# Kernel tuning notes

Hardware: AMD Instinct MI355X
Metric: run time of the kernel (lower is better)

The kernel has to match this reference:

```python
import jax, jax.numpy as jnp
import numpy as np
from jax.scipy.special import logsumexp


def setup_inputs() -> dict:
    key = jax.random.key(0)
    B, C, H, W = 2, 32, 128, 128
    sizes = [(H, W)] + [(H // 2, W // 2)] * 4
    ks = iter(jax.random.split(key, 32))
    inp = {}
    for t, (hh, ww) in enumerate(sizes):
        inp[f"unary_h{t}"] = jax.random.normal(next(ks), (B, C, hh, ww), jnp.float32)
        inp[f"unary_v{t}"] = jax.random.normal(next(ks), (B, C, hh, ww), jnp.float32)
        inp[f"pairwise_h{t}"] = 0.1 * jax.random.normal(next(ks), (B, C, C, hh, ww - 1), jnp.float32)
        inp[f"pairwise_v{t}"] = 0.1 * jax.random.normal(next(ks), (B, C, C, hh - 1, ww), jnp.float32)
    inp["gamma"] = jnp.ones((1,), jnp.float32)
    return inp


def _chain_marginals(unary, pairwise, gamma):
    """Entropy-smoothed max-product marginals along the LAST axis.
    unary: [B,C,L,T], pairwise: [B,C,C,L,T-1] (pairwise[b,i,j,l,t] couples state i at t with j at t+1).
    Returns soft marginals [B,C,L,T] (softmax over C per position)."""
    u = jnp.transpose(unary, (3, 0, 2, 1))        # [T,B,L,C]
    pw = jnp.transpose(pairwise, (4, 0, 3, 1, 2))  # [T-1,B,L,C,C]
    inv_g = 1.0 / gamma

    def fwd_step(f, xs):
        u_t, pw_t = xs
        f_new = u_t + gamma * logsumexp(f[..., :, None] * inv_g + pw_t * inv_g, axis=-2)
        return f_new, f_new

    _, f_rest = jax.lax.scan(fwd_step, u[0], (u[1:], pw))
    f = jnp.concatenate([u[:1], f_rest], axis=0)

    def bwd_step(bb, xs):
        u_t, pw_t = xs
        b_new = u_t + gamma * logsumexp(bb[..., None, :] * inv_g + pw_t * inv_g, axis=-1)
        return b_new, b_new

    _, b_rest = jax.lax.scan(bwd_step, u[-1], (u[:-1][::-1], pw[::-1]))
    b = jnp.concatenate([u[-1:], b_rest], axis=0)[::-1]

    marg = jax.nn.softmax((f + b - u) * inv_g, axis=-1)  # [T,B,L,C]
    return jnp.transpose(marg, (1, 3, 2, 0))             # [B,C,L,T]


def _dp_pair(uh, uv, ph, pv, g):
    # horizontal chains (along W) with unary_h, vertical chains (along H) with unary_v
    mh = _chain_marginals(uh, ph, g)
    mv = _chain_marginals(uv.swapaxes(2, 3), pv.swapaxes(3, 4), g).swapaxes(2, 3)
    return mh, mv


def _scatter_up(m, stride, i, j, H, W):
    # max_unpool2d with the structured indices: m[y,x] -> (i + y*stride, j + x*stride), then crop/pad to (H,W)
    b, c, h_, w_ = m.shape
    up = jnp.zeros((b, c, h_ * stride, w_ * stride), m.dtype).at[:, :, i::stride, j::stride].set(m)
    up = up[:, :, :H, :W]
    ph, pw = H - up.shape[2], W - up.shape[3]
    if ph > 0 or pw > 0:
        up = jnp.pad(up, ((0, 0), (0, 0), (0, max(ph, 0)), (0, max(pw, 0))))
    return up


def reference(unary_h0, unary_h1, unary_h2, unary_h3, unary_h4,
              unary_v0, unary_v1, unary_v2, unary_v3, unary_v4,
              pairwise_h0, pairwise_h1, pairwise_h2, pairwise_h3, pairwise_h4,
              pairwise_v0, pairwise_v1, pairwise_v2, pairwise_v3, pairwise_v4,
              gamma):
    uh = [unary_h0, unary_h1, unary_h2, unary_h3, unary_h4]
    uv = [unary_v0, unary_v1, unary_v2, unary_v3, unary_v4]
    ph = [pairwise_h0, pairwise_h1, pairwise_h2, pairwise_h3, pairwise_h4]
    pv = [pairwise_v0, pairwise_v1, pairwise_v2, pairwise_v3, pairwise_v4]
    g = jnp.clip(gamma.reshape(()), 0.01)  # learned gamma, clamped min 0.01

    H, W = uh[0].shape[2], uh[0].shape[3]
    alpha = 1.0 / W if W > H else 1.0 / H

    mh0, mv0 = _dp_pair(uh[0], uv[0], ph[0], pv[0], g)
    marg_hs, marg_vs = [mh0], [mv0]
    mh_acc, mv_acc = mh0, mv0

    stride, cnt = 2, 1  # step_size = 1 default -> one extra scale with a 2x2 shifted grid
    for i in range(stride):
        for j in range(stride):
            m_h, m_v = _dp_pair(uh[cnt], uv[cnt], ph[cnt], pv[cnt], g)
            marg_hs.append(m_h)
            marg_vs.append(m_v)
            mh_acc = mh_acc + _scatter_up(m_h, stride, i, j, H, W)
            mv_acc = mv_acc + _scatter_up(m_v, stride, i, j, H, W)
            cnt += 1

    num_pairwise_terms = 2
    avg = (mh_acc + mv_acc) / (num_pairwise_terms * 2)

    new_uh0 = uh[0] - alpha * (marg_hs[0] - avg)
    new_uv0 = uv[0] - alpha * (marg_vs[0] - avg)
    # fine-scale unary updates (computed for faithfulness; gradients flow through avg)
    cnt = 1
    new_uh_fine, new_uv_fine = [], []
    for i in range(stride):
        for j in range(stride):
            new_uh_fine.append(uh[cnt] - alpha * (marg_hs[cnt] - avg[:, :, i::stride, j::stride]))
            new_uv_fine.append(uv[cnt] - alpha * (marg_vs[cnt] - avg[:, :, i::stride, j::stride]))
            cnt += 1

    main = jnp.stack([new_uh0, new_uv0, mh_acc, mv_acc], axis=0)  # [4,B,C,H,W]
    return main
```

## Files before the change

### kernel.cpp

```cpp
#include <hip/hip_runtime.h>
#include <stdint.h>

#define TC 4
#define CHUNK_BYTES 8192
#define CHUNK_F4 512

static __device__ __forceinline__ float lse16x2(const float* v, float igl2, float gln2, float uval)
{
  float a0=fmaxf(v[0],v[8]), a1=fmaxf(v[1],v[9]), a2=fmaxf(v[2],v[10]), a3=fmaxf(v[3],v[11]);
  float a4=fmaxf(v[4],v[12]),a5=fmaxf(v[5],v[13]),a6=fmaxf(v[6],v[14]),a7=fmaxf(v[7],v[15]);
  float b0=fmaxf(a0,a4), b1=fmaxf(a1,a5), b2=fmaxf(a2,a6), b3=fmaxf(a3,a7);
  float m = fmaxf(fmaxf(b0,b1), fmaxf(b2,b3));
  float e0 = exp2f((v[0]-m)*igl2) + exp2f((v[1]-m)*igl2);
  float e1 = exp2f((v[2]-m)*igl2) + exp2f((v[3]-m)*igl2);
  float e2 = exp2f((v[4]-m)*igl2) + exp2f((v[5]-m)*igl2);
  float e3 = exp2f((v[6]-m)*igl2) + exp2f((v[7]-m)*igl2);
  float e4 = exp2f((v[8]-m)*igl2) + exp2f((v[9]-m)*igl2);
  float e5 = exp2f((v[10]-m)*igl2) + exp2f((v[11]-m)*igl2);
  float e6 = exp2f((v[12]-m)*igl2) + exp2f((v[13]-m)*igl2);
  float e7 = exp2f((v[14]-m)*igl2) + exp2f((v[15]-m)*igl2);
  float s = ((e0+e1)+(e2+e3)) + ((e4+e5)+(e6+e7));
  float mo = __shfl_xor(m, 32);
  float m2 = fmaxf(m, mo);
  float sadj = s * exp2f((m - m2) * igl2);
  float stot = sadj + __shfl_xor(sadj, 32);
  return uval + m2 + gln2 * __log2f(stot);
}

static __device__ __forceinline__ float softmax32(float z)
{
  float zm = z;
  zm = fmaxf(zm, __shfl_xor(zm, 16));
  zm = fmaxf(zm, __shfl_xor(zm, 8));
  zm = fmaxf(zm, __shfl_xor(zm, 4));
  zm = fmaxf(zm, __shfl_xor(zm, 2));
  zm = fmaxf(zm, __shfl_xor(zm, 1));
  float p = exp2f((z - zm) * 1.4426950408889634f);
  float ps = p;
  ps += __shfl_xor(ps, 16);
  ps += __shfl_xor(ps, 8);
  ps += __shfl_xor(ps, 4);
  ps += __shfl_xor(ps, 2);
  ps += __shfl_xor(ps, 1);
  return p / ps;
}

static __device__ __forceinline__ uint32_t pkbf(float a, float b)
{
  uint32_t ua = __float_as_uint(a), ub = __float_as_uint(b);
  ua = (ua + 0x7FFFu + ((ua >> 16) & 1u)) >> 16;
  ub = (ub + 0x7FFFu + ((ub >> 16) & 1u)) & 0xFFFF0000u;
  return ua | ub;
}

struct TSeg { const float* pw; uint16_t* PT; int L, Tt, Tpad, fStride, Xtot, dirV, blockBase, nx, ny; };
struct TTable { TSeg s[10]; int nseg; };
struct USeg { const float* U; float* Ut; int fs, nx, ny, L, T, dirV, blockBase; };
struct UTable { USeg s[10]; int nseg; };
struct DSeg { const uint16_t* PT; const float* Ut; float* F; float* B; int chainBase, T, Tt, Tpad; };
struct DTable { DSeg s[10]; int nseg; };
struct MSeg { const float* F; const float* B; const float* Ut; float* out; int L, T, dirV, blockBase, nrx, nfx; };
struct MTable { MSeg s[10]; int nseg; };

__global__ __launch_bounds__(256) void k_transpose_all(TTable tbl)
{
  __shared__ uint16_t tile[128][128];
  int bid = blockIdx.x;
  int k = 0;
  for (int q = 1; q < tbl.nseg; q++) if (bid >= tbl.s[q].blockBase) k = q;
  TSeg sg = tbl.s[k];
  int r = bid - sg.blockBase;
  int jg = r & 7; r >>= 3;
  int w = r % sg.nx; int tmp = r / sg.nx;
  int fixed = tmp % sg.ny;
  int b = tmp / sg.ny;
  int j0 = jg * 4;
  int g = fixed * sg.fStride;
  int a = g & 31;
  int xbase = w * 128 - a;
  if (xbase >= sg.Xtot) return;
  int tid = threadIdx.x;
  int kx = tid & 31, psub = tid >> 5;
  int pstride = sg.L * sg.Tt;
  int clampMax = 2048 * pstride - 4;
  int jthr = j0 + (psub & 3);
  int swj = (jthr >> 1) & 3;
  int gp0 = ((psub >> 2) << 5) + jthr;
  int idx0 = ((b << 10) + gp0) * pstride + (g - a) + (w << 7) + (kx << 2);
  const float* pw = sg.pw;
  #pragma unroll
  for (int hp = 0; hp < 2; hp++) {
    float4 st[8];
    #pragma unroll
    for (int q = 0; q < 8; q++) {
      int batch = hp * 8 + q;
      int idx = idx0 + batch * (pstride << 6);
      idx = idx > clampMax ? clampMax : idx;
      st[q] = *(const float4*)(pw + idx);
    }
    #pragma unroll
    for (int q = 0; q < 8; q++) {
      int batch = hp * 8 + q;
      int i = 2 * batch + (psub >> 2);
      int sw = swj ^ (((i >> 3) & 3) << 2);
      int pl = batch * 8 + psub;
      uint32_t pk0 = pkbf(st[q].x, st[q].y);
      uint32_t pk1 = pkbf(st[q].z, st[q].w);
      if (sw & 1) { uint32_t tswp = pk0; pk0 = pk1; pk1 = tswp; }
      *(uint2*)((unsigned char*)tile + pl * 256 + 8 * (kx ^ (sw >> 1))) = make_uint2(pk0, pk1);
    }
  }
  __syncthreads();
  uint32_t* PTd = (uint32_t*)sg.PT;
  #pragma unroll
  for (int w8 = 0; w8 < 8; w8++) {
    int gidx = w8 * 256 + tid;
    int xs = gidx >> 4;
    int q = gidx & 15;
    int xv = xbase + xs;
    if (xv < 0 || xv >= sg.Xtot) continue;
    int jl = q >> 2, j = j0 + jl;
    int perm3 = (j >> 1) & 7;
    int swjW = (j >> 1) & 3;
    uint32_t pk[4];
    #pragma unroll
    for (int e = 0; e < 4; e++) {
      int wd = ((q & 3) << 2) + e;
      int pos = wd >> 1, pr = wd & 1;
      int i0 = ((pos ^ perm3) << 2) + pr * 2;
      int sw = swjW ^ (((i0 >> 3) & 3) << 2);
      int c = (xs >> 1) ^ sw;
      int u16c = (c << 1) | (xs & 1);
      int r0 = (i0 << 2) + jl;
      uint32_t v0 = tile[r0][u16c];
      uint32_t v1 = tile[r0 + 4][u16c];
      pk[e] = v0 | (v1 << 16);
    }
    int chain, tsl;
    if (sg.dirV) { chain = b * sg.Xtot + xv; tsl = fixed; }
    else         { chain = b * sg.ny + fixed; tsl = xv; }
    *(uint4*)&PTd[((size_t)chain * sg.Tpad + tsl) * 512 + j * 16 + (q & 3) * 4] =
        make_uint4(pk[0], pk[1], pk[2], pk[3]);
  }
}

__global__ __launch_bounds__(256) void k_ut_all(UTable tbl)
{
  __shared__ float tile[32][33];
  int bid = blockIdx.x;
  int k = 0;
  for (int q = 1; q < tbl.nseg; q++) if (bid >= tbl.s[q].blockBase) k = q;
  USeg sg = tbl.s[k];
  int r = bid - sg.blockBase;
  int bx = r % sg.nx; int tmp = r / sg.nx;
  int fixed = tmp % sg.ny;
  int b = tmp / sg.ny;
  int tid = threadIdx.x;
  size_t LT = (size_t)sg.L * sg.T;
  int x0 = bx * 32;
  int xx = tid & 31;
  #pragma unroll
  for (int it = 0; it < 4; it++) {
    int c = (tid >> 5) + it * 8;
    tile[xx][c] = sg.U[(size_t)b * 32 * LT + (size_t)c * LT + (size_t)fixed * sg.fs + x0 + xx];
  }
  __syncthreads();
  int cw = tid & 31;
  #pragma unroll
  for (int it = 0; it < 4; it++) {
    int xw = (tid >> 5) + it * 8;
    int chain = sg.dirV ? b * sg.L + x0 + xw : b * sg.L + fixed;
    int tIdx  = sg.dirV ? fixed : x0 + xw;
    sg.Ut[((size_t)chain * sg.T + tIdx) * 32 + cw] = tile[xw][cw];
  }
}

__global__ __launch_bounds__(64) void k_dp_all(DTable tbl, const float* __restrict__ gamma, int nDP)
{
  __shared__ __align__(16) unsigned char lds[2 * CHUNK_BYTES];
  int bid = blockIdx.x;
  int isB = (bid >= nDP) ? 1 : 0;
  bid -= isB * nDP;
  int k = 0;
  for (int q = 1; q < tbl.nseg; q++) if (bid >= tbl.s[q].chainBase) k = q;
  DSeg sg = tbl.s[k];
  int chain = bid - sg.chainBase;
  int T = sg.T, Tt = sg.Tt;
  int tid = threadIdx.x, j = tid & 31, h = tid >> 5;
  float g = fmaxf(gamma[0], 0.01f);
  float igl2 = (1.0f / g) * 1.4426950408889634f;
  float gln2 = g * 0.6931471805599453f;
  const float* Utc = sg.Ut + (size_t)chain * T * 32;
  float* Oc = (isB ? sg.B : sg.F) + (size_t)chain * T * 32;
  const float4* src = (const float4*)(sg.PT + (size_t)chain * sg.Tpad * 1024);
  int nch = sg.Tpad / TC;
  int perm3 = (j >> 1) & 7;
  int gbase = h * 48;
  float4 stg[8];
  if (!isB) {
    float cur = Utc[j];
    if (h == 0) Oc[j] = cur;
    #pragma unroll
    for (int q = 0; q < 8; q++) stg[q] = src[q * 64 + tid];
    int buf = 0;
    for (int ch = 0; ch < nch; ch++) {
      float4* dst = (float4*)(lds + buf * CHUNK_BYTES);
      #pragma unroll
      for (int q = 0; q < 8; q++) dst[q * 64 + tid] = stg[q];
      if (ch + 1 < nch) {
        const float4* s2 = src + (size_t)(ch + 1) * CHUNK_F4;
        #pragma unroll
        for (int q = 0; q < 8; q++) stg[q] = s2[q * 64 + tid];
      }
      #pragma unroll
      for (int ss = 0; ss < TC; ss++) {
        int s = ch * TC + ss;
        if (s >= Tt) break;
        const uint32_t* sl = (const uint32_t*)(lds + buf * CHUNK_BYTES + ss * 2048);
        float v[16];
        #pragma unroll
        for (int rr = 0; rr < 4; rr++) {
          int pos = (4 * h + rr) ^ perm3;
          uint2 dv = *(const uint2*)&sl[j * 16 + pos * 2];
          v[rr * 4 + 0] = __uint_as_float(dv.x << 16);
          v[rr * 4 + 1] = __uint_as_float(dv.x & 0xFFFF0000u);
          v[rr * 4 + 2] = __uint_as_float(dv.y << 16);
          v[rr * 4 + 3] = __uint_as_float(dv.y & 0xFFFF0000u);
        }
        #pragma unroll
        for (int q = 0; q < 16; q++) v[q] += __shfl(cur, gbase + q);
        float uval = Utc[(size_t)(s + 1) * 32 + j];
        cur = lse16x2(v, igl2, gln2, uval);
        if (h == 0) Oc[(size_t)(s + 1) * 32 + j] = cur;
      }
      buf ^= 1;
    }
  } else {
    int p2i = j >> 2, pri = (j >> 1) & 1, loi = j & 1;
    float cur = Utc[(size_t)(T - 1) * 32 + j];
    if (h == 0) Oc[(size_t)(T - 1) * 32 + j] = cur;
    {
      const float4* s2 = src + (size_t)(nch - 1) * CHUNK_F4;
      #pragma unroll
      for (int q = 0; q < 8; q++) stg[q] = s2[q * 64 + tid];
    }
    int buf = 0;
    for (int ch = nch - 1; ch >= 0; ch--) {
      float4* dst = (float4*)(lds + buf * CHUNK_BYTES);
      #pragma unroll
      for (int q = 0; q < 8; q++) dst[q * 64 + tid] = stg[q];
      if (ch > 0) {
        const float4* s2 = src + (size_t)(ch - 1) * CHUNK_F4;
        #pragma unroll
        for (int q = 0; q < 8; q++) stg[q] = s2[q * 64 + tid];
      }
      #pragma unroll
      for (int ss = TC - 1; ss >= 0; ss--) {
        int s = ch * TC + ss;
        if (s >= Tt) continue;
        const uint16_t* row16 = (const uint16_t*)(lds + buf * CHUNK_BYTES + ss * 2048);
        float v[16];
        #pragma unroll
        for (int jj = 0; jj < 16; jj++) {
          int u16idx = (16 * h + jj) * 32 + ((p2i ^ (jj >> 1)) * 2 + pri) * 2 + loi;
          v[jj] = __uint_as_float((uint32_t)row16[u16idx] << 16);
        }
        #pragma unroll
        for (int q = 0; q < 16; q++) v[q] += __shfl(cur, gbase + q);
        float uval = Utc[(size_t)s * 32 + j];
        cur = lse16x2(v, igl2, gln2, uval);
        if (h == 0) Oc[(size_t)s * 32 + j] = cur;
      }
      buf ^= 1;
    }
  }
}

__global__ __launch_bounds__(256) void k_marg_all(MTable tbl, const float* __restrict__ gamma)
{
  __shared__ float sm[32][33];
  int bid = blockIdx.x;
  int k = 0;
  for (int q = 1; q < tbl.nseg; q++) if (bid >= tbl.s[q].blockBase) k = q;
  MSeg sg = tbl.s[k];
  int r = bid - sg.blockBase;
  int rx = r % sg.nrx; int tmp = r / sg.nrx;
  int fx = tmp % sg.nfx; int b = tmp / sg.nfx;
  int tid = threadIdx.x;
  float g = fmaxf(gamma[0], 0.01f);
  float ig = 1.0f / g;
  int c = tid & 31;
  int L = sg.L, T = sg.T;
  size_t LT = (size_t)L * T;
  int RA = sg.dirV ? L : T;
  int r0 = rx * 32;
  #pragma unroll
  for (int pass = 0; pass < 4; pass++) {
    int rr = (tid >> 5) + pass * 8;
    int rowAxis = r0 + rr;
    int chain = sg.dirV ? b * L + rowAxis : b * L + fx;
    int t = sg.dirV ? fx : rowAxis;
    size_t idx = ((size_t)chain * T + t) * 32 + c;
    float z = (sg.F[idx] + sg.B[idx] - sg.Ut[idx]) * ig;
    sm[rr][c] = softmax32(z);
  }
  __syncthreads();
  size_t obase = (size_t)b * 32 * LT + (size_t)fx * RA + r0;
  #pragma unroll
  for (int pass = 0; pass < 4; pass++) {
    int cc = (tid >> 5) + pass * 8;
    sg.out[obase + (size_t)cc * LT + (tid & 31)] = sm[tid & 31][cc];
  }
}

__global__ __launch_bounds__(256) void k_combine(
    const float* __restrict__ uh0, const float* __restrict__ uv0,
    const float* __restrict__ MB, float* __restrict__ out)
{
  int idx = blockIdx.x * 256 + threadIdx.x;
  int x = idx & 127, y = (idx >> 7) & 127;
  int bc = idx >> 14;
  float mh0 = MB[idx];
  float mv0 = MB[1048576 + idx];
  int cnt = 1 + ((y & 1) << 1) + (x & 1);
  int coff = bc * 4096 + ((y >> 1) << 6) + (x >> 1);
  const float* cb = MB + 2097152 + (size_t)(cnt - 1) * 524288;
  float mhc = cb[coff];
  float mvc = cb[262144 + coff];
  float mha = mh0 + mhc, mva = mv0 + mvc;
  float avg = (mha + mva) * 0.25f;
  const float A = 0.0078125f;
  out[idx]           = uh0[idx] - A * (mh0 - avg);
  out[1048576 + idx] = uv0[idx] - A * (mv0 - avg);
  out[2097152 + idx] = mha;
  out[3145728 + idx] = mva;
}

static void fill_tseg(TSeg& t, const float* pw, uint16_t* PT, int L, int T, int dirV, int blockBase)
{
  int Tt = T - 1;
  t.pw = pw; t.PT = PT;
  t.L = L; t.Tt = Tt; t.Tpad = T;
  t.fStride = dirV ? L : Tt;
  t.Xtot = dirV ? L : Tt;
  t.dirV = dirV;
  int pad = (t.fStride & 31) ? 31 : 0;
  t.nx = (t.Xtot + pad + 127) / 128;
  t.ny = dirV ? Tt : L;
  t.blockBase = blockBase;
}

extern "C" void kernel_launch(void* const* d_in, const int* in_sizes, int n_in,
                              void* d_out, int out_size, void* d_ws, size_t ws_size,
                              hipStream_t stream)
{
  (void)in_sizes; (void)n_in; (void)out_size;
  const float* gamma = (const float*)d_in[20];
  unsigned char* ws = (unsigned char*)d_ws;

  int segL[10], segT[10];
  const float* segPW[10]; const float* segUU[10];
  size_t segMG[10];
  for (int lvl = 0; lvl < 5; lvl++) {
    int H = lvl ? 64 : 128, W = H;
    int si = lvl * 2;
    segL[si] = H; segT[si] = W;
    segPW[si] = (const float*)d_in[lvl * 4 + 2];
    segUU[si] = (const float*)d_in[lvl * 4 + 0];
    segL[si + 1] = W; segT[si + 1] = H;
    segPW[si + 1] = (const float*)d_in[lvl * 4 + 3];
    segUU[si + 1] = (const float*)d_in[lvl * 4 + 1];
    if (lvl == 0) { segMG[0] = 0; segMG[1] = 1048576; }
    else { segMG[si] = 2097152 + (size_t)(lvl - 1) * 524288; segMG[si + 1] = segMG[si] + 262144; }
  }

  const size_t NEED = 318767104ull;
  if (ws_size >= NEED) {
    uint16_t* PT0 = (uint16_t*)ws;
    float* MARG = (float*)ws;
    float* F0  = (float*)(ws + 268435456ull);
    float* B0  = (float*)(ws + 285212672ull);
    float* Ut0 = (float*)(ws + 301989888ull);

    TTable tt; UTable ut; DTable dt; MTable mt;
    tt.nseg = 10; ut.nseg = 10; dt.nseg = 10; mt.nseg = 10;
    size_t ptOff = 0, fuOff = 0;
    int tB = 0, uB = 0, cB = 0, mB = 0;
    for (int s = 0; s < 10; s++) {
      int dirV = s & 1;
      int L = segL[s], T = segT[s];
      int chains = 2 * L;
      fill_tseg(tt.s[s], segPW[s], PT0 + ptOff, L, T, dirV, tB);
      tB += 2 * tt.s[s].ny * tt.s[s].nx * 8;
      USeg& u = ut.s[s];
      u.U = segUU[s]; u.Ut = Ut0 + fuOff;
      u.fs = dirV ? L : T;
      u.nx = (dirV ? L : T) / 32;
      u.ny = dirV ? T : L;
      u.L = L; u.T = T; u.dirV = dirV;
      u.blockBase = uB;
      uB += u.nx * u.ny * 2;
      DSeg& d = dt.s[s];
      d.PT = PT0 + ptOff; d.Ut = Ut0 + fuOff;
      d.F = F0 + fuOff; d.B = B0 + fuOff;
      d.chainBase = cB; d.T = T; d.Tt = T - 1; d.Tpad = T;
      cB += chains;
      MSeg& m = mt.s[s];
      m.F = F0 + fuOff; m.B = B0 + fuOff; m.Ut = Ut0 + fuOff;
      m.out = MARG + segMG[s];
      m.L = L; m.T = T; m.dirV = dirV;
      m.blockBase = mB;
      m.nrx = (dirV ? L : T) / 32;
      m.nfx = dirV ? T : L;
      mB += 2 * m.nfx * m.nrx;
      ptOff += (size_t)chains * T * 1024;
      fuOff += (size_t)chains * T * 32;
    }
    k_transpose_all<<<tB, 256, 0, stream>>>(tt);
    k_ut_all<<<uB, 256, 0, stream>>>(ut);
    k_dp_all<<<2 * cB, 64, 0, stream>>>(dt, gamma, cB);
    k_marg_all<<<mB, 256, 0, stream>>>(mt, gamma);
    k_combine<<<4096, 256, 0, stream>>>((const float*)d_in[0], (const float*)d_in[1],
                                        MARG, (float*)d_out);
  } else {
    uint16_t* PT0 = (uint16_t*)ws;
    float* F0  = (float*)(ws + 67108864ull);
    float* B0  = (float*)(ws + 71303168ull);
    float* Ut0 = (float*)(ws + 75497472ull);
    float* MARG = (float*)(ws + 79691776ull);
    for (int s = 0; s < 10; s++) {
      int dirV = s & 1;
      int L = segL[s], T = segT[s];
      int chains = 2 * L;
      TTable tt; tt.nseg = 1;
      fill_tseg(tt.s[0], segPW[s], PT0, L, T, dirV, 0);
      int nb = 2 * tt.s[0].ny * tt.s[0].nx * 8;
      k_transpose_all<<<nb, 256, 0, stream>>>(tt);
      UTable ut; ut.nseg = 1;
      USeg& u = ut.s[0];
      u.U = segUU[s]; u.Ut = Ut0;
      u.fs = dirV ? L : T;
      u.nx = (dirV ? L : T) / 32;
      u.ny = dirV ? T : L;
      u.L = L; u.T = T; u.dirV = dirV; u.blockBase = 0;
      int ub = u.nx * u.ny * 2;
      k_ut_all<<<ub, 256, 0, stream>>>(ut);
      DTable dt; dt.nseg = 1;
      DSeg& d = dt.s[0];
      d.PT = PT0; d.Ut = Ut0; d.F = F0; d.B = B0;
      d.chainBase = 0; d.T = T; d.Tt = T - 1; d.Tpad = T;
      k_dp_all<<<2 * chains, 64, 0, stream>>>(dt, gamma, chains);
      MTable mt; mt.nseg = 1;
      MSeg& m = mt.s[0];
      m.F = F0; m.B = B0; m.Ut = Ut0; m.out = MARG + segMG[s];
      m.L = L; m.T = T; m.dirV = dirV; m.blockBase = 0;
      m.nrx = (dirV ? L : T) / 32;
      m.nfx = dirV ? T : L;
      int mb = 2 * m.nfx * m.nrx;
      k_marg_all<<<mb, 256, 0, stream>>>(mt, gamma);
    }
    k_combine<<<4096, 256, 0, stream>>>((const float*)d_in[0], (const float*)d_in[1],
                                        MARG, (float*)d_out);
  }
}
```

Measured before the change: 435.5 us.

## Vectorize stores across kernels and batch DP outputs through LDS staging

```diff
diff --git a/kernel.cpp b/kernel.cpp
--- a/kernel.cpp
+++ b/kernel.cpp
@@ -1,9 +1,9 @@
 #include <hip/hip_runtime.h>
 #include <stdint.h>
 
-#define TC 4
-#define CHUNK_BYTES 8192
-#define CHUNK_F4 512
+#define TC 2
+#define CHUNK_BYTES 4096
+#define CHUNK_F4 256
 
 static __device__ __forceinline__ float lse16x2(const float* v, float igl2, float gln2, float uval)
 {
@@ -165,19 +165,18 @@
     tile[xx][c] = sg.U[(size_t)b * 32 * LT + (size_t)c * LT + (size_t)fixed * sg.fs + x0 + xx];
   }
   __syncthreads();
-  int cw = tid & 31;
-  #pragma unroll
-  for (int it = 0; it < 4; it++) {
-    int xw = (tid >> 5) + it * 8;
-    int chain = sg.dirV ? b * sg.L + x0 + xw : b * sg.L + fixed;
-    int tIdx  = sg.dirV ? fixed : x0 + xw;
-    sg.Ut[((size_t)chain * sg.T + tIdx) * 32 + cw] = tile[xw][cw];
-  }
+  int xw = tid >> 3;
+  int ci = (tid & 7) * 4;
+  int chain = sg.dirV ? b * sg.L + x0 + xw : b * sg.L + fixed;
+  int tIdx  = sg.dirV ? fixed : x0 + xw;
+  float4 vv = make_float4(tile[xw][ci], tile[xw][ci + 1], tile[xw][ci + 2], tile[xw][ci + 3]);
+  *(float4*)&sg.Ut[((size_t)chain * sg.T + tIdx) * 32 + ci] = vv;
 }
 
 __global__ __launch_bounds__(64) void k_dp_all(DTable tbl, const float* __restrict__ gamma, int nDP)
 {
-  __shared__ __align__(16) unsigned char lds[2 * CHUNK_BYTES];
+  __shared__ __align__(16) unsigned char lds[2 * CHUNK_BYTES + 1024];
+  float* f_out = (float*)(lds + 2 * CHUNK_BYTES);
   int bid = blockIdx.x;
   int isB = (bid >= nDP) ? 1 : 0;
   bid -= isB * nDP;
@@ -196,21 +195,21 @@
   int nch = sg.Tpad / TC;
   int perm3 = (j >> 1) & 7;
   int gbase = h * 48;
-  float4 stg[8];
+  float4 stg[4];
   if (!isB) {
     float cur = Utc[j];
-    if (h == 0) Oc[j] = cur;
+    if (h == 0) f_out[j] = cur;
     #pragma unroll
-    for (int q = 0; q < 8; q++) stg[q] = src[q * 64 + tid];
+    for (int q = 0; q < 4; q++) stg[q] = src[q * 64 + tid];
     int buf = 0;
     for (int ch = 0; ch < nch; ch++) {
       float4* dst = (float4*)(lds + buf * CHUNK_BYTES);
       #pragma unroll
-      for (int q = 0; q < 8; q++) dst[q * 64 + tid] = stg[q];
+      for (int q = 0; q < 4; q++) dst[q * 64 + tid] = stg[q];
       if (ch + 1 < nch) {
         const float4* s2 = src + (size_t)(ch + 1) * CHUNK_F4;
         #pragma unroll
-        for (int q = 0; q < 8; q++) stg[q] = s2[q * 64 + tid];
+        for (int q = 0; q < 4; q++) stg[q] = s2[q * 64 + tid];
       }
       #pragma unroll
       for (int ss = 0; ss < TC; ss++) {
@@ -229,30 +228,35 @@
         }
         #pragma unroll
         for (int q = 0; q < 16; q++) v[q] += __shfl(cur, gbase + q);
-        float uval = Utc[(size_t)(s + 1) * 32 + j];
+        int t = s + 1;
+        float uval = Utc[(size_t)t * 32 + j];
         cur = lse16x2(v, igl2, gln2, uval);
-        if (h == 0) Oc[(size_t)(s + 1) * 32 + j] = cur;
+        if (h == 0) f_out[(t & 7) * 32 + j] = cur;
+        if ((t & 7) == 7) {
+          float4 vv = *(float4*)&f_out[tid * 4];
+          *(float4*)&Oc[(size_t)(t - 7) * 32 + tid * 4] = vv;
+        }
       }
       buf ^= 1;
     }
   } else {
     int p2i = j >> 2, pri = (j >> 1) & 1, loi = j & 1;
     float cur = Utc[(size_t)(T - 1) * 32 + j];
-    if (h == 0) Oc[(size_t)(T - 1) * 32 + j] = cur;
+    if (h == 0) f_out[7 * 32 + j] = cur;
     {
       const float4* s2 = src + (size_t)(nch - 1) * CHUNK_F4;
       #pragma unroll
-      for (int q = 0; q < 8; q++) stg[q] = s2[q * 64 + tid];
+      for (int q = 0; q < 4; q++) stg[q] = s2[q * 64 + tid];
     }
     int buf = 0;
     for (int ch = nch - 1; ch >= 0; ch--) {
       float4* dst = (float4*)(lds + buf * CHUNK_BYTES);
       #pragma unroll
-      for (int q = 0; q < 8; q++) dst[q * 64 + tid] = stg[q];
+      for (int q = 0; q < 4; q++) dst[q * 64 + tid] = stg[q];
       if (ch > 0) {
         const float4* s2 = src + (size_t)(ch - 1) * CHUNK_F4;
         #pragma unroll
-        for (int q = 0; q < 8; q++) stg[q] = s2[q * 64 + tid];
+        for (int q = 0; q < 4; q++) stg[q] = s2[q * 64 + tid];
       }
       #pragma unroll
       for (int ss = TC - 1; ss >= 0; ss--) {
@@ -269,7 +273,11 @@
         for (int q = 0; q < 16; q++) v[q] += __shfl(cur, gbase + q);
         float uval = Utc[(size_t)s * 32 + j];
         cur = lse16x2(v, igl2, gln2, uval);
-        if (h == 0) Oc[(size_t)s * 32 + j] = cur;
+        if (h == 0) f_out[(s & 7) * 32 + j] = cur;
+        if ((s & 7) == 0) {
+          float4 vv = *(float4*)&f_out[tid * 4];
+          *(float4*)&Oc[(size_t)s * 32 + tid * 4] = vv;
+        }
       }
       buf ^= 1;
     }
@@ -305,35 +313,53 @@
     sm[rr][c] = softmax32(z);
   }
   __syncthreads();
+  int cc = tid >> 3;
+  int xl = (tid & 7) * 4;
   size_t obase = (size_t)b * 32 * LT + (size_t)fx * RA + r0;
-  #pragma unroll
-  for (int pass = 0; pass < 4; pass++) {
-    int cc = (tid >> 5) + pass * 8;
-    sg.out[obase + (size_t)cc * LT + (tid & 31)] = sm[tid & 31][cc];
-  }
+  float4 vv = make_float4(sm[xl][cc], sm[xl + 1][cc], sm[xl + 2][cc], sm[xl + 3][cc]);
+  *(float4*)&sg.out[obase + (size_t)cc * LT + xl] = vv;
 }
 
 __global__ __launch_bounds__(256) void k_combine(
     const float* __restrict__ uh0, const float* __restrict__ uv0,
     const float* __restrict__ MB, float* __restrict__ out)
 {
-  int idx = blockIdx.x * 256 + threadIdx.x;
-  int x = idx & 127, y = (idx >> 7) & 127;
-  int bc = idx >> 14;
-  float mh0 = MB[idx];
-  float mv0 = MB[1048576 + idx];
-  int cnt = 1 + ((y & 1) << 1) + (x & 1);
+  int t4 = blockIdx.x * 256 + threadIdx.x;
+  int base = t4 * 4;
+  int x = base & 127, y = (base >> 7) & 127;
+  int bc = base >> 14;
+  float4 mh0 = *(const float4*)&MB[base];
+  float4 mv0 = *(const float4*)&MB[1048576 + base];
+  int ce = 1 + ((y & 1) << 1);
   int coff = bc * 4096 + ((y >> 1) << 6) + (x >> 1);
-  const float* cb = MB + 2097152 + (size_t)(cnt - 1) * 524288;
-  float mhc = cb[coff];
-  float mvc = cb[262144 + coff];
-  float mha = mh0 + mhc, mva = mv0 + mvc;
-  float avg = (mha + mva) * 0.25f;
+  const float* cbE = MB + 2097152 + (size_t)(ce - 1) * 524288;
+  const float* cbO = cbE + 524288;
+  float2 mhcE = *(const float2*)&cbE[coff];
+  float2 mhcO = *(const float2*)&cbO[coff];
+  float2 mvcE = *(const float2*)&cbE[262144 + coff];
+  float2 mvcO = *(const float2*)&cbO[262144 + coff];
+  float4 u_h = *(const float4*)&uh0[base];
+  float4 u_v = *(const float4*)&uv0[base];
+  float mh[4] = {mh0.x, mh0.y, mh0.z, mh0.w};
+  float mv[4] = {mv0.x, mv0.y, mv0.z, mv0.w};
+  float uh[4] = {u_h.x, u_h.y, u_h.z, u_h.w};
+  float uv[4] = {u_v.x, u_v.y, u_v.z, u_v.w};
+  float mhc[4] = {mhcE.x, mhcO.x, mhcE.y, mhcO.y};
+  float mvc[4] = {mvcE.x, mvcO.x, mvcE.y, mvcO.y};
+  float o0[4], o1[4], o2[4], o3[4];
   const float A = 0.0078125f;
-  out[idx]           = uh0[idx] - A * (mh0 - avg);
-  out[1048576 + idx] = uv0[idx] - A * (mv0 - avg);
-  out[2097152 + idx] = mha;
-  out[3145728 + idx] = mva;
+  #pragma unroll
+  for (int e = 0; e < 4; e++) {
+    float mha = mh[e] + mhc[e], mva = mv[e] + mvc[e];
+    float avg = (mha + mva) * 0.25f;
+    o0[e] = uh[e] - A * (mh[e] - avg);
+    o1[e] = uv[e] - A * (mv[e] - avg);
+    o2[e] = mha; o3[e] = mva;
+  }
+  *(float4*)&out[base]           = make_float4(o0[0], o0[1], o0[2], o0[3]);
+  *(float4*)&out[1048576 + base] = make_float4(o1[0], o1[1], o1[2], o1[3]);
+  *(float4*)&out[2097152 + base] = make_float4(o2[0], o2[1], o2[2], o2[3]);
+  *(float4*)&out[3145728 + base] = make_float4(o3[0], o3[1], o3[2], o3[3]);
 }
 
 static void fill_tseg(TSeg& t, const float* pw, uint16_t* PT, int L, int T, int dirV, int blockBase)
@@ -420,7 +446,7 @@
     k_ut_all<<<uB, 256, 0, stream>>>(ut);
     k_dp_all<<<2 * cB, 64, 0, stream>>>(dt, gamma, cB);
     k_marg_all<<<mB, 256, 0, stream>>>(mt, gamma);
-    k_combine<<<4096, 256, 0, stream>>>((const float*)d_in[0], (const float*)d_in[1],
+    k_combine<<<1024, 256, 0, stream>>>((const float*)d_in[0], (const float*)d_in[1],
                                         MARG, (float*)d_out);
   } else {
     uint16_t* PT0 = (uint16_t*)ws;
@@ -459,7 +485,7 @@
       int mb = 2 * m.nfx * m.nrx;
       k_marg_all<<<mb, 256, 0, stream>>>(mt, gamma);
     }
-    k_combine<<<4096, 256, 0, stream>>>((const float*)d_in[0], (const float*)d_in[1],
+    k_combine<<<1024, 256, 0, stream>>>((const float*)d_in[0], (const float*)d_in[1],
                                         MARG, (float*)d_out);
   }
 }
```

Result: faster. 426.7 us (-2.0%).
